# Kernel tuning notes

Hardware: AMD Instinct MI355X
Metric: run time of the kernel (lower is better)

The kernel has to match this reference:

```python
import jax, jax.numpy as jnp
import numpy as np

N = 30000
E = 480000
C_IN, H = 16, 4
NEG_SLOPE = 0.2  # PyG GATv2Conv default negative_slope


def gatv2(x, src, dst, Wl, bl, Wr, br, att, bias, heads, outc, concat, n):
    # PyG GATv2Conv (share_weights=False): e_ij = att . leaky_relu(Wl x_j + Wr x_i)
    xl = (x @ Wl + bl).reshape(n, heads, outc)   # source transform
    xr = (x @ Wr + br).reshape(n, heads, outc)   # target transform
    e = jax.nn.leaky_relu(xl[src] + xr[dst], NEG_SLOPE)        # [E,H,C]
    logits = jnp.einsum('ehc,hc->eh', e, att)                  # [E,H]
    m = jax.lax.stop_gradient(jax.ops.segment_max(logits, dst, num_segments=n))
    ex = jnp.exp(logits - m[dst])
    denom = jax.ops.segment_sum(ex, dst, num_segments=n)
    alpha = ex / denom[dst]                                    # scatter-softmax over in-edges
    out = jax.ops.segment_sum(alpha[:, :, None] * xl[src], dst, num_segments=n)  # [N,H,C]
    out = out.reshape(n, heads * outc) if concat else out.mean(axis=1)
    return out + bias


def setup_inputs() -> dict:
    key = jax.random.key(0)
    ks = jax.random.split(key, 16)
    s = 0.05
    inp = {
        'x': jax.random.uniform(ks[0], (N, C_IN), dtype=jnp.float32),
        'edge_index': jax.random.randint(ks[1], (2, E), 0, N, dtype=jnp.int32),
        'lower_bound': jnp.zeros((C_IN,), jnp.float32),
        'upper_bound': jnp.ones((C_IN,), jnp.float32),
        # Layer 1: GATv2Conv(16 -> 32 per head, heads=4, concat=True) => 128
        'W1l': jax.random.normal(ks[2], (C_IN, H * 32), jnp.float32) * s,
        'b1l': jnp.zeros((H * 32,), jnp.float32),
        'W1r': jax.random.normal(ks[3], (C_IN, H * 32), jnp.float32) * s,
        'b1r': jnp.zeros((H * 32,), jnp.float32),
        'att1': jax.random.normal(ks[4], (H, 32), jnp.float32) * s,
        'bias1': jnp.zeros((H * 32,), jnp.float32),
        # Layer 2: GATv2Conv(128 -> 64 per head, heads=4, concat=False) => 64
        'W2l': jax.random.normal(ks[5], (128, H * 64), jnp.float32) * s,
        'b2l': jnp.zeros((H * 64,), jnp.float32),
        'W2r': jax.random.normal(ks[6], (128, H * 64), jnp.float32) * s,
        'b2r': jnp.zeros((H * 64,), jnp.float32),
        'att2': jax.random.normal(ks[7], (H, 64), jnp.float32) * s,
        'bias2': jnp.zeros((64,), jnp.float32),
        # Final linear head 64 -> 5
        'W3': jax.random.normal(ks[8], (64, 5), jnp.float32) * s,
        'b3': jnp.zeros((5,), jnp.float32),
    }
    return inp


def reference(x, edge_index, lower_bound, upper_bound,
              W1l, b1l, W1r, b1r, att1, bias1,
              W2l, b2l, W2r, b2r, att2, bias2,
              W3, b3):
    n = x.shape[0]
    # min-max normalization
    y = (x - lower_bound) / (upper_bound - lower_bound)
    # add self loops (PyG GATv2Conv default add_self_loops=True)
    loops = jnp.tile(jnp.arange(n, dtype=edge_index.dtype)[None, :], (2, 1))
    ei = jnp.concatenate([edge_index, loops], axis=1)
    src, dst = ei[0], ei[1]
    y = gatv2(y, src, dst, W1l, b1l, W1r, b1r, att1, bias1, H, 32, True, n)
    y = jax.nn.relu(y)
    y = gatv2(y, src, dst, W2l, b2l, W2r, b2r, att2, bias2, H, 64, False, n)
    y = jax.nn.relu(y)
    y = y @ W3 + b3
    return jax.nn.sigmoid(y)
```

## Files before the change

kernel.cpp:

```cpp
#include <hip/hip_runtime.h>

#define H 4
#define D1 128
#define D2 256
#define CIN 16
#define SLOPE 0.2f
#define LOG2E 1.4426950408889634f

typedef short short8v __attribute__((ext_vector_type(8)));
typedef float float4v __attribute__((ext_vector_type(4)));
typedef float float2v __attribute__((ext_vector_type(2)));

__device__ __forceinline__ float bflo(unsigned u) { return __uint_as_float(u << 16); }
__device__ __forceinline__ float bfdirty(unsigned u) { return __uint_as_float(u); }
__device__ __forceinline__ unsigned short f2bf(float f) {
    unsigned int u = __float_as_uint(f);
    u += 0x7FFFu + ((u >> 16) & 1u);
    return (unsigned short)(u >> 16);
}
__device__ __forceinline__ unsigned short f2fp8x2(float a, float b) {
    return (unsigned short)__builtin_amdgcn_cvt_pk_fp8_f32(a, b, 0, false);
}

__device__ __forceinline__ float dpp_sum16(float x) {
    float t;
    t = __int_as_float(__builtin_amdgcn_mov_dpp(__float_as_int(x), 0xB1, 0xF, 0xF, true));
    x += t;
    t = __int_as_float(__builtin_amdgcn_mov_dpp(__float_as_int(x), 0x4E, 0xF, 0xF, true));
    x += t;
    t = __int_as_float(__builtin_amdgcn_mov_dpp(__float_as_int(x), 0x141, 0xF, 0xF, true));
    x += t;
    t = __int_as_float(__builtin_amdgcn_mov_dpp(__float_as_int(x), 0x140, 0xF, 0xF, true));
    x += t;
    return x;
}

__global__ void k_hist(const int* __restrict__ ei, int E, int ET,
                       int* __restrict__ deg) {
    int idx = blockIdx.x * blockDim.x + threadIdx.x;
    if (idx >= ET) return;
    int dst = (idx < E) ? ei[E + idx] : idx - E;
    atomicAdd(&deg[dst], 1);
}

__global__ __launch_bounds__(1024) void k_scan_one(
        const int* __restrict__ deg, int* __restrict__ rp,
        int* __restrict__ cur, int n) {
    __shared__ int wsum[16];
    int t = threadIdx.x;
    int lane = t & 63, w = t >> 6;
    int base = t * 32;
    int vals[32];
    const int4* dp = (const int4*)deg;
#pragma unroll
    for (int q = 0; q < 8; ++q) {
        int4 v = dp[(base >> 2) + q];
        vals[4 * q + 0] = v.x; vals[4 * q + 1] = v.y;
        vals[4 * q + 2] = v.z; vals[4 * q + 3] = v.w;
    }
    int loc[32];
    int s = 0;
#pragma unroll
    for (int k = 0; k < 32; ++k) {
        int idx = base + k;
        int v = (idx < n) ? vals[k] : 0;
        loc[k] = s;
        s += v;
    }
    int inc = s;
#pragma unroll
    for (int off = 1; off < 64; off <<= 1) {
        int u = __shfl_up(inc, off, 64);
        if (lane >= off) inc += u;
    }
    int excl = inc - s;
    if (lane == 63) wsum[w] = inc;
    __syncthreads();
    if (w == 0) {
        int v = (lane < 16) ? wsum[lane] : 0;
        int winc = v;
#pragma unroll
        for (int off = 1; off < 16; off <<= 1) {
            int u = __shfl_up(winc, off, 64);
            if (lane >= off) winc += u;
        }
        if (lane < 16) wsum[lane] = winc - v;
    }
    __syncthreads();
    int offw = wsum[w] + excl;
#pragma unroll
    for (int q = 0; q < 8; ++q) {
        int i0 = base + 4 * q;
        if (i0 + 3 < n) {
            *(int4*)(rp + i0) = make_int4(offw + loc[4 * q + 0], offw + loc[4 * q + 1],
                                          offw + loc[4 * q + 2], offw + loc[4 * q + 3]);
            *(int4*)(cur + i0) = make_int4(0, 0, 0, 0);
        } else {
#pragma unroll
            for (int e = 0; e < 4; ++e) {
                int idx = i0 + e;
                if (idx < n) { rp[idx] = offw + loc[4 * q + e]; cur[idx] = 0; }
            }
        }
    }
}

__global__ void k_fill(const int* __restrict__ ei, int E, int ET,
                       const int* __restrict__ rp, int* __restrict__ cur,
                       int* __restrict__ eord) {
    int idx = blockIdx.x * blockDim.x + threadIdx.x;
    if (idx >= ET) return;
    int src, dst;
    if (idx < E) { src = ei[idx]; dst = ei[E + idx]; }
    else         { src = dst = idx - E; }
    int pos = atomicAdd(&cur[dst], 1);
    eord[rp[dst] + pos] = src;
}

__global__ __launch_bounds__(256) void k_prep(
        const float* __restrict__ x, const float* __restrict__ lb,
        const float* __restrict__ ub,
        const float* __restrict__ Wl, const float* __restrict__ bl,
        const float* __restrict__ Wr, const float* __restrict__ br,
        unsigned char* __restrict__ xl8, float* __restrict__ xr,
        const float* __restrict__ W2l, const float* __restrict__ W2r,
        unsigned short* __restrict__ W2t,
        int* __restrict__ deg, int n, int B1) {
    __shared__ float Wls[CIN][D1];
    __shared__ float Wrs[CIN][D1];
    __shared__ float ys[16][CIN];
    int b = blockIdx.x;
    int t = threadIdx.x;
    if (b >= B1) {
        int rb = b - B1;
        if (rb < 256) {
            int idx = rb * 256 + t;
            int k = idx >> 9, c = idx & 511;
            float v = (c < 256) ? W2l[k * 256 + c] : W2r[k * 256 + (c - 256)];
            W2t[(size_t)c * 128 + k] = f2bf(v);
        } else {
            int idx = (rb - 256) * 256 + t;
            if (idx < n) deg[idx] = 0;
        }
        return;
    }
    int i0 = b * 16;
#pragma unroll
    for (int i = 0; i < 8; ++i) {
        int flat = t + 256 * i;
        int k = flat >> 7, c = flat & 127;
        Wls[k][c] = Wl[k * D1 + c];
        Wrs[k][c] = Wr[k * D1 + c];
    }
    {
        int node = t >> 4, k = t & 15;
        int gi = i0 + node;
        float xv = (gi < n) ? x[(size_t)gi * CIN + k] : 0.f;
        ys[node][k] = (xv - lb[k]) / (ub[k] - lb[k]);
    }
    __syncthreads();
    int c = t & 127;
    bool left = t < 128;
    const float (*Ws)[D1] = left ? Wls : Wrs;
    float bias = left ? bl[c] : br[c];
    for (int j = 0; j < 16; ++j) {
        float acc = bias;
#pragma unroll
        for (int k = 0; k < CIN; ++k) acc += ys[j][k] * Ws[k][c];
        int gi = i0 + j;
        float other = __shfl_xor(acc, 1);
        if (gi < n) {
            if (left) {
                if (!(c & 1))
                    *(unsigned short*)(xl8 + (size_t)gi * D1 + c) = f2fp8x2(acc, other);
            } else {
                xr[(size_t)gi * D1 + c] = acc;
            }
        }
    }
}

__global__ __launch_bounds__(256) void k_lin2_mfma(
        const unsigned short* __restrict__ h1b,
        const unsigned short* __restrict__ W2t,
        const float* __restrict__ b2l, const float* __restrict__ b2r,
        unsigned char* __restrict__ xl2,
        unsigned short* __restrict__ xr2,
        int n) {
    __shared__ unsigned short At[128 * 128];
    __shared__ unsigned short Bt[128 * 128];
    int t = threadIdx.x;
    int row0 = blockIdx.x * 128;
    int col0 = blockIdx.y * 128;

    {
        int r = t >> 1, hh = (t & 1) * 64;
        bool ok = (row0 + r) < n;
        const unsigned short* gA = h1b + (size_t)(row0 + r) * 128 + hh;
        const unsigned short* gB = W2t + (size_t)(col0 + r) * 128 + hh;
#pragma unroll
        for (int i = 0; i < 8; ++i) {
            uint4 vA = ok ? *(const uint4*)(gA + i * 8) : make_uint4(0, 0, 0, 0);
            uint4 vB = *(const uint4*)(gB + i * 8);
            int col = hh + i * 8;
            int idx = (r * 128 + col) ^ ((r & 15) << 3);
            *(uint4*)&At[idx] = vA;
            *(uint4*)&Bt[idx] = vB;
        }
    }
    __syncthreads();

    int w = t >> 6, l = t & 63;
    int wr = w >> 1, wc = w & 1;
    float4v acc[4][4];
#pragma unroll
    for (int m = 0; m < 4; ++m)
#pragma unroll
        for (int nn = 0; nn < 4; ++nn) acc[m][nn] = (float4v)0.f;

#pragma unroll
    for (int ks = 0; ks < 4; ++ks) {
        int kb = ks * 32 + ((l >> 4) << 3);
        short8v a[4], b[4];
#pragma unroll
        for (int m = 0; m < 4; ++m) {
            int r = wr * 64 + m * 16 + (l & 15);
            a[m] = *(const short8v*)&At[(r * 128 + kb) ^ ((r & 15) << 3)];
        }
#pragma unroll
        for (int nn = 0; nn < 4; ++nn) {
            int c = wc * 64 + nn * 16 + (l & 15);
            b[nn] = *(const short8v*)&Bt[(c * 128 + kb) ^ ((c & 15) << 3)];
        }
#pragma unroll
        for (int m = 0; m < 4; ++m)
#pragma unroll
            for (int nn = 0; nn < 4; ++nn)
                acc[m][nn] = __builtin_amdgcn_mfma_f32_16x16x32_bf16(
                    a[m], b[nn], acc[m][nn], 0, 0, 0);
    }

    if (col0 < 256) {
        const float* bp = b2l;
        int cb = col0;
#pragma unroll
        for (int nn = 0; nn < 4; ++nn) {
            int colc = cb + wc * 64 + nn * 16 + (l & 15);
            float bv = bp[colc];
#pragma unroll
            for (int m = 0; m < 4; ++m) {
                int rbase = row0 + wr * 64 + m * 16 + ((l >> 4) << 2);
#pragma unroll
                for (int r = 0; r < 4; ++r) {
                    int row = rbase + r;
                    float val = acc[m][nn][r] + bv;
                    float other = __shfl_xor(val, 1);
                    if (!(l & 1) && row < n)
                        *(unsigned short*)(xl2 + (size_t)row * 256 + colc) =
                            f2fp8x2(val, other);
                }
            }
        }
    } else {
        const float* bp = b2r;
        int cb = col0 - 256;
#pragma unroll
        for (int nn = 0; nn < 4; ++nn) {
            int colc = cb + wc * 64 + nn * 16 + (l & 15);
            float bv = bp[colc];
#pragma unroll
            for (int m = 0; m < 4; ++m) {
                int rbase = row0 + wr * 64 + m * 16 + ((l >> 4) << 2);
#pragma unroll
                for (int r = 0; r < 4; ++r) {
                    int row = rbase + r;
                    if (row < n)
                        xr2[(size_t)row * 256 + colc] = f2bf(acc[m][nn][r] + bv);
                }
            }
        }
    }
}

__global__ __launch_bounds__(256) void k_agg1(
        const unsigned char* __restrict__ xl8, const float* __restrict__ xr,
        const float* __restrict__ att, const float* __restrict__ bias,
        const int* __restrict__ rp, const int* __restrict__ deg,
        const int* __restrict__ eord, unsigned short* __restrict__ h1b, int n) {
    int t = threadIdx.x;
    int node = blockIdx.x * 4 + (t >> 6);
    int l = t & 63;
    int nd = (node < n) ? node : n - 1;
    float2 xrv = *(const float2*)(xr + (size_t)nd * D1 + 2 * l);
    float2 av  = *(const float2*)(att + 2 * l);
    av.x *= LOG2E; av.y *= LOG2E;
    int start = __builtin_amdgcn_readfirstlane(rp[nd]);
    int cnt   = (node < n) ? deg[nd] : 0;
    cnt = __builtin_amdgcn_readfirstlane(cnt);
    const unsigned short* xlp = (const unsigned short*)xl8;
    float d = 0.f, a0 = 0.f, a1 = 0.f;
    int cnt4 = cnt & ~3;
    unsigned r0, r1, r2, r3;
    if (cnt4 > 0) {
        int i0 = eord[start + 0], i1 = eord[start + 1];
        int i2 = eord[start + 2], i3 = eord[start + 3];
        r0 = xlp[(size_t)i0 * 64 + l]; r1 = xlp[(size_t)i1 * 64 + l];
        r2 = xlp[(size_t)i2 * 64 + l]; r3 = xlp[(size_t)i3 * 64 + l];
    }
    for (int j = 0; j < cnt4; j += 4) {
        unsigned p0 = r0, p1 = r1, p2 = r2, p3 = r3;
        int jn = j + 4;
        if (jn < cnt4) {
            int i0 = eord[start + jn + 0], i1 = eord[start + jn + 1];
            int i2 = eord[start + jn + 2], i3 = eord[start + jn + 3];
            r0 = xlp[(size_t)i0 * 64 + l]; r1 = xlp[(size_t)i1 * 64 + l];
            r2 = xlp[(size_t)i2 * 64 + l]; r3 = xlp[(size_t)i3 * 64 + l];
        }
        float2v f0 = __builtin_amdgcn_cvt_pk_f32_fp8(p0, false);
        float2v f1 = __builtin_amdgcn_cvt_pk_f32_fp8(p1, false);
        float2v f2 = __builtin_amdgcn_cvt_pk_f32_fp8(p2, false);
        float2v f3 = __builtin_amdgcn_cvt_pk_f32_fp8(p3, false);
        float v, lg0, lg1, lg2, lg3;
        v = f0.x + xrv.x; v = fmaxf(v, SLOPE * v); lg0  = av.x * v;
        v = f0.y + xrv.y; v = fmaxf(v, SLOPE * v); lg0 += av.y * v;
        v = f1.x + xrv.x; v = fmaxf(v, SLOPE * v); lg1  = av.x * v;
        v = f1.y + xrv.y; v = fmaxf(v, SLOPE * v); lg1 += av.y * v;
        v = f2.x + xrv.x; v = fmaxf(v, SLOPE * v); lg2  = av.x * v;
        v = f2.y + xrv.y; v = fmaxf(v, SLOPE * v); lg2 += av.y * v;
        v = f3.x + xrv.x; v = fmaxf(v, SLOPE * v); lg3  = av.x * v;
        v = f3.y + xrv.y; v = fmaxf(v, SLOPE * v); lg3 += av.y * v;
        lg0 = dpp_sum16(lg0); lg1 = dpp_sum16(lg1);
        lg2 = dpp_sum16(lg2); lg3 = dpp_sum16(lg3);
        float e0 = exp2f(lg0), e1 = exp2f(lg1);
        float e2 = exp2f(lg2), e3 = exp2f(lg3);
        d += (e0 + e1) + (e2 + e3);
        a0 += e0 * f0.x + e1 * f1.x + e2 * f2.x + e3 * f3.x;
        a1 += e0 * f0.y + e1 * f1.y + e2 * f2.y + e3 * f3.y;
    }
    for (int j = cnt4; j < cnt; ++j) {
        int s0 = eord[start + j];
        unsigned p0 = xlp[(size_t)s0 * 64 + l];
        float2v f0 = __builtin_amdgcn_cvt_pk_f32_fp8(p0, false);
        float v, lg0;
        v = f0.x + xrv.x; v = fmaxf(v, SLOPE * v); lg0  = av.x * v;
        v = f0.y + xrv.y; v = fmaxf(v, SLOPE * v); lg0 += av.y * v;
        lg0 = dpp_sum16(lg0);
        float e0 = exp2f(lg0);
        d += e0;
        a0 += e0 * f0.x;
        a1 += e0 * f0.y;
    }
    if (node < n) {
        float inv = 1.f / d;
        float o0 = fmaxf(a0 * inv + bias[2 * l + 0], 0.f);
        float o1 = fmaxf(a1 * inv + bias[2 * l + 1], 0.f);
        ((unsigned*)h1b)[(size_t)node * 64 + l] =
            ((unsigned)f2bf(o1) << 16) | f2bf(o0);
    }
}

__global__ __launch_bounds__(256) void k_agg2(
        const unsigned char* __restrict__ xl8, const unsigned short* __restrict__ xr,
        const float* __restrict__ att, const float* __restrict__ b2,
        const float* __restrict__ W3, const float* __restrict__ b3,
        const int* __restrict__ rp, const int* __restrict__ deg,
        const int* __restrict__ eord, float* __restrict__ out, int n) {
    int t = threadIdx.x;
    int node = blockIdx.x * 4 + (t >> 6);
    int l = t & 63;
    int nd = (node < n) ? node : n - 1;
    const uint2* xrp = (const uint2*)xr;
    uint2 xru = xrp[(size_t)nd * 64 + l];
    float4 xrv = make_float4(bflo(xru.x), bfdirty(xru.x), bflo(xru.y), bfdirty(xru.y));
    float4 av  = *(const float4*)(att + 4 * l);
    av.x *= LOG2E; av.y *= LOG2E; av.z *= LOG2E; av.w *= LOG2E;
    int start = __builtin_amdgcn_readfirstlane(rp[nd]);
    int cnt   = (node < n) ? deg[nd] : 0;
    cnt = __builtin_amdgcn_readfirstlane(cnt);
    const unsigned* xlp = (const unsigned*)xl8;
    float d = 0.f, a0 = 0.f, a1 = 0.f, a2 = 0.f, a3 = 0.f;
    int cnt4 = cnt & ~3;
    unsigned r0, r1, r2, r3;
    if (cnt4 > 0) {
        int i0 = eord[start + 0], i1 = eord[start + 1];
        int i2 = eord[start + 2], i3 = eord[start + 3];
        r0 = xlp[(size_t)i0 * 64 + l]; r1 = xlp[(size_t)i1 * 64 + l];
        r2 = xlp[(size_t)i2 * 64 + l]; r3 = xlp[(size_t)i3 * 64 + l];
    }
    for (int j = 0; j < cnt4; j += 4) {
        unsigned p0 = r0, p1 = r1, p2 = r2, p3 = r3;
        int jn = j + 4;
        if (jn < cnt4) {
            int i0 = eord[start + jn + 0], i1 = eord[start + jn + 1];
            int i2 = eord[start + jn + 2], i3 = eord[start + jn + 3];
            r0 = xlp[(size_t)i0 * 64 + l]; r1 = xlp[(size_t)i1 * 64 + l];
            r2 = xlp[(size_t)i2 * 64 + l]; r3 = xlp[(size_t)i3 * 64 + l];
        }
        float2v lo0 = __builtin_amdgcn_cvt_pk_f32_fp8(p0, false);
        float2v hi0 = __builtin_amdgcn_cvt_pk_f32_fp8(p0, true);
        float2v lo1 = __builtin_amdgcn_cvt_pk_f32_fp8(p1, false);
        float2v hi1 = __builtin_amdgcn_cvt_pk_f32_fp8(p1, true);
        float2v lo2 = __builtin_amdgcn_cvt_pk_f32_fp8(p2, false);
        float2v hi2 = __builtin_amdgcn_cvt_pk_f32_fp8(p2, true);
        float2v lo3 = __builtin_amdgcn_cvt_pk_f32_fp8(p3, false);
        float2v hi3 = __builtin_amdgcn_cvt_pk_f32_fp8(p3, true);
        float v, lg0, lg1, lg2, lg3;
        v = lo0.x + xrv.x; v = fmaxf(v, SLOPE * v); lg0  = av.x * v;
        v = lo0.y + xrv.y; v = fmaxf(v, SLOPE * v); lg0 += av.y * v;
        v = hi0.x + xrv.z; v = fmaxf(v, SLOPE * v); lg0 += av.z * v;
        v = hi0.y + xrv.w; v = fmaxf(v, SLOPE * v); lg0 += av.w * v;
        v = lo1.x + xrv.x; v = fmaxf(v, SLOPE * v); lg1  = av.x * v;
        v = lo1.y + xrv.y; v = fmaxf(v, SLOPE * v); lg1 += av.y * v;
        v = hi1.x + xrv.z; v = fmaxf(v, SLOPE * v); lg1 += av.z * v;
        v = hi1.y + xrv.w; v = fmaxf(v, SLOPE * v); lg1 += av.w * v;
        v = lo2.x + xrv.x; v = fmaxf(v, SLOPE * v); lg2  = av.x * v;
        v = lo2.y + xrv.y; v = fmaxf(v, SLOPE * v); lg2 += av.y * v;
        v = hi2.x + xrv.z; v = fmaxf(v, SLOPE * v); lg2 += av.z * v;
        v = hi2.y + xrv.w; v = fmaxf(v, SLOPE * v); lg2 += av.w * v;
        v = lo3.x + xrv.x; v = fmaxf(v, SLOPE * v); lg3  = av.x * v;
        v = lo3.y + xrv.y; v = fmaxf(v, SLOPE * v); lg3 += av.y * v;
        v = hi3.x + xrv.z; v = fmaxf(v, SLOPE * v); lg3 += av.z * v;
        v = hi3.y + xrv.w; v = fmaxf(v, SLOPE * v); lg3 += av.w * v;
        lg0 = dpp_sum16(lg0); lg1 = dpp_sum16(lg1);
        lg2 = dpp_sum16(lg2); lg3 = dpp_sum16(lg3);
        float e0 = exp2f(lg0), e1 = exp2f(lg1);
        float e2 = exp2f(lg2), e3 = exp2f(lg3);
        d += (e0 + e1) + (e2 + e3);
        a0 += e0 * lo0.x + e1 * lo1.x + e2 * lo2.x + e3 * lo3.x;
        a1 += e0 * lo0.y + e1 * lo1.y + e2 * lo2.y + e3 * lo3.y;
        a2 += e0 * hi0.x + e1 * hi1.x + e2 * hi2.x + e3 * hi3.x;
        a3 += e0 * hi0.y + e1 * hi1.y + e2 * hi2.y + e3 * hi3.y;
    }
    for (int j = cnt4; j < cnt; ++j) {
        int s0 = eord[start + j];
        unsigned p0 = xlp[(size_t)s0 * 64 + l];
        float2v lo0 = __builtin_amdgcn_cvt_pk_f32_fp8(p0, false);
        float2v hi0 = __builtin_amdgcn_cvt_pk_f32_fp8(p0, true);
        float v, lg0;
        v = lo0.x + xrv.x; v = fmaxf(v, SLOPE * v); lg0  = av.x * v;
        v = lo0.y + xrv.y; v = fmaxf(v, SLOPE * v); lg0 += av.y * v;
        v = hi0.x + xrv.z; v = fmaxf(v, SLOPE * v); lg0 += av.z * v;
        v = hi0.y + xrv.w; v = fmaxf(v, SLOPE * v); lg0 += av.w * v;
        lg0 = dpp_sum16(lg0);
        float e0 = exp2f(lg0);
        d += e0;
        a0 += e0 * lo0.x; a1 += e0 * lo0.y; a2 += e0 * hi0.x; a3 += e0 * hi0.y;
    }
    float inv = 1.f / d;
    float v0 = a0 * inv, v1 = a1 * inv, v2 = a2 * inv, v3 = a3 * inv;
    v0 += __shfl_xor(v0, 16); v1 += __shfl_xor(v1, 16);
    v2 += __shfl_xor(v2, 16); v3 += __shfl_xor(v3, 16);
    v0 += __shfl_xor(v0, 32); v1 += __shfl_xor(v1, 32);
    v2 += __shfl_xor(v2, 32); v3 += __shfl_xor(v3, 32);
    int c0 = 4 * (l & 15);
    v0 = fmaxf(0.25f * v0 + b2[c0 + 0], 0.f);
    v1 = fmaxf(0.25f * v1 + b2[c0 + 1], 0.f);
    v2 = fmaxf(0.25f * v2 + b2[c0 + 2], 0.f);
    v3 = fmaxf(0.25f * v3 + b2[c0 + 3], 0.f);
    float p0, p1, p2, p3, p4;
    {
        const float* w0 = W3 + (c0 + 0) * 5;
        const float* w1 = W3 + (c0 + 1) * 5;
        const float* w2 = W3 + (c0 + 2) * 5;
        const float* w3 = W3 + (c0 + 3) * 5;
        p0 = v0 * w0[0] + v1 * w1[0] + v2 * w2[0] + v3 * w3[0];
        p1 = v0 * w0[1] + v1 * w1[1] + v2 * w2[1] + v3 * w3[1];
        p2 = v0 * w0[2] + v1 * w1[2] + v2 * w2[2] + v3 * w3[2];
        p3 = v0 * w0[3] + v1 * w1[3] + v2 * w2[3] + v3 * w3[3];
        p4 = v0 * w0[4] + v1 * w1[4] + v2 * w2[4] + v3 * w3[4];
    }
    p0 = dpp_sum16(p0); p1 = dpp_sum16(p1); p2 = dpp_sum16(p2);
    p3 = dpp_sum16(p3); p4 = dpp_sum16(p4);
    if (l == 0 && node < n) {
        float* o = out + (size_t)node * 5;
        o[0] = 1.f / (1.f + __expf(-(p0 + b3[0])));
        o[1] = 1.f / (1.f + __expf(-(p1 + b3[1])));
        o[2] = 1.f / (1.f + __expf(-(p2 + b3[2])));
        o[3] = 1.f / (1.f + __expf(-(p3 + b3[3])));
        o[4] = 1.f / (1.f + __expf(-(p4 + b3[4])));
    }
}

extern "C" void kernel_launch(void* const* d_in, const int* in_sizes, int n_in,
                              void* d_out, int out_size, void* d_ws, size_t ws_size,
                              hipStream_t stream) {
    const float* x     = (const float*)d_in[0];
    const int*   ei    = (const int*)d_in[1];
    const float* lb    = (const float*)d_in[2];
    const float* ub    = (const float*)d_in[3];
    const float* W1l   = (const float*)d_in[4];
    const float* b1l   = (const float*)d_in[5];
    const float* W1r   = (const float*)d_in[6];
    const float* b1r   = (const float*)d_in[7];
    const float* att1  = (const float*)d_in[8];
    const float* bias1 = (const float*)d_in[9];
    const float* W2l   = (const float*)d_in[10];
    const float* b2l   = (const float*)d_in[11];
    const float* W2r   = (const float*)d_in[12];
    const float* b2r   = (const float*)d_in[13];
    const float* att2  = (const float*)d_in[14];
    const float* bias2 = (const float*)d_in[15];
    const float* W3    = (const float*)d_in[16];
    const float* b3    = (const float*)d_in[17];

    int n  = in_sizes[0] / CIN;
    int E  = in_sizes[1] / 2;
    int ET = E + n;

    char* ws = (char*)d_ws;
    size_t off = 0;
    auto alloc = [&](size_t nbytes) {
        void* p = ws + off;
        off += (nbytes + 255) & ~(size_t)255;
        return p;
    };
    unsigned char*  xl1 = (unsigned char*)alloc((size_t)n * D1);
    float*          xr1 = (float*)alloc((size_t)n * D1 * 4);
    unsigned short* h1b = (unsigned short*)alloc((size_t)n * D1 * 2);
    unsigned char*  xl2 = (unsigned char*)alloc((size_t)n * D2);
    unsigned short* xr2 = (unsigned short*)alloc((size_t)n * D2 * 2);
    unsigned short* W2t = (unsigned short*)alloc((size_t)512 * 128 * 2);
    int* deg  = (int*)alloc((size_t)n * 4 + 8192);
    int* cur  = (int*)alloc((size_t)n * 4);
    int* rp   = (int*)alloc((size_t)n * 4);
    int* eord = (int*)alloc((size_t)ET * 4);

    int B1 = (n + 15) / 16;
    int BZ = (n + 255) / 256;
    k_prep<<<B1 + 256 + BZ, 256, 0, stream>>>(
        x, lb, ub, W1l, b1l, W1r, b1r, xl1, xr1, W2l, W2r, W2t, deg, n, B1);

    k_hist<<<(ET + 255) / 256, 256, 0, stream>>>(ei, E, ET, deg);
    k_scan_one<<<1, 1024, 0, stream>>>(deg, rp, cur, n);
    k_fill<<<(ET + 255) / 256, 256, 0, stream>>>(ei, E, ET, rp, cur, eord);

    k_agg1<<<(n + 3) / 4, 256, 0, stream>>>(xl1, xr1, att1, bias1, rp, deg,
                                            eord, h1b, n);

    dim3 g2((n + 127) / 128, 4);
    k_lin2_mfma<<<g2, 256, 0, stream>>>(h1b, W2t, b2l, b2r, xl2, xr2, n);
    k_agg2<<<(n + 3) / 4, 256, 0, stream>>>(xl2, xr2, att2, bias2, W3, b3,
                                            rp, deg, eord, (float*)d_out, n);
}
```

Baseline: 182.4 us.

## Switch gather features from fp8 to fp16 and use packed half math in aggregation

```diff
diff --git a/kernel.cpp b/kernel.cpp
--- a/kernel.cpp
+++ b/kernel.cpp
@@ -9,17 +9,28 @@
 
 typedef short short8v __attribute__((ext_vector_type(8)));
 typedef float float4v __attribute__((ext_vector_type(4)));
-typedef float float2v __attribute__((ext_vector_type(2)));
-
-__device__ __forceinline__ float bflo(unsigned u) { return __uint_as_float(u << 16); }
-__device__ __forceinline__ float bfdirty(unsigned u) { return __uint_as_float(u); }
+typedef __fp16 half2v __attribute__((ext_vector_type(2)));
+
 __device__ __forceinline__ unsigned short f2bf(float f) {
     unsigned int u = __float_as_uint(f);
     u += 0x7FFFu + ((u >> 16) & 1u);
     return (unsigned short)(u >> 16);
 }
-__device__ __forceinline__ unsigned short f2fp8x2(float a, float b) {
-    return (unsigned short)__builtin_amdgcn_cvt_pk_fp8_f32(a, b, 0, false);
+__device__ __forceinline__ half2v pkrtz(float a, float b) {
+    return __builtin_amdgcn_cvt_pkrtz(a, b);
+}
+__device__ __forceinline__ half2v h2_from_u32(unsigned u) {
+    return __builtin_bit_cast(half2v, u);
+}
+__device__ __forceinline__ unsigned u32_from_h2(half2v h) {
+    return __builtin_bit_cast(unsigned, h);
+}
+__device__ __forceinline__ float fdot2(half2v a, half2v b, float c) {
+#if __has_builtin(__builtin_amdgcn_fdot2)
+    return __builtin_amdgcn_fdot2(a, b, c, false);
+#else
+    return c + (float)a.x * (float)b.x + (float)a.y * (float)b.y;
+#endif
 }
 
 __device__ __forceinline__ float dpp_sum16(float x) {
@@ -122,7 +133,7 @@
         const float* __restrict__ ub,
         const float* __restrict__ Wl, const float* __restrict__ bl,
         const float* __restrict__ Wr, const float* __restrict__ br,
-        unsigned char* __restrict__ xl8, float* __restrict__ xr,
+        unsigned short* __restrict__ xl16, unsigned short* __restrict__ xr16,
         const float* __restrict__ W2l, const float* __restrict__ W2r,
         unsigned short* __restrict__ W2t,
         int* __restrict__ deg, int n, int B1) {
@@ -163,20 +174,15 @@
     bool left = t < 128;
     const float (*Ws)[D1] = left ? Wls : Wrs;
     float bias = left ? bl[c] : br[c];
+    unsigned short* obuf = left ? xl16 : xr16;
     for (int j = 0; j < 16; ++j) {
         float acc = bias;
 #pragma unroll
         for (int k = 0; k < CIN; ++k) acc += ys[j][k] * Ws[k][c];
         int gi = i0 + j;
         float other = __shfl_xor(acc, 1);
-        if (gi < n) {
-            if (left) {
-                if (!(c & 1))
-                    *(unsigned short*)(xl8 + (size_t)gi * D1 + c) = f2fp8x2(acc, other);
-            } else {
-                xr[(size_t)gi * D1 + c] = acc;
-            }
-        }
+        if (gi < n && !(c & 1))
+            *(unsigned*)(obuf + (size_t)gi * D1 + c) = u32_from_h2(pkrtz(acc, other));
     }
 }
 
@@ -184,7 +190,7 @@
         const unsigned short* __restrict__ h1b,
         const unsigned short* __restrict__ W2t,
         const float* __restrict__ b2l, const float* __restrict__ b2r,
-        unsigned char* __restrict__ xl2,
+        unsigned short* __restrict__ xl2,
         unsigned short* __restrict__ xr2,
         int n) {
     __shared__ unsigned short At[128 * 128];
@@ -240,50 +246,31 @@
                     a[m], b[nn], acc[m][nn], 0, 0, 0);
     }
 
-    if (col0 < 256) {
-        const float* bp = b2l;
-        int cb = col0;
-#pragma unroll
-        for (int nn = 0; nn < 4; ++nn) {
-            int colc = cb + wc * 64 + nn * 16 + (l & 15);
-            float bv = bp[colc];
-#pragma unroll
-            for (int m = 0; m < 4; ++m) {
-                int rbase = row0 + wr * 64 + m * 16 + ((l >> 4) << 2);
-#pragma unroll
-                for (int r = 0; r < 4; ++r) {
-                    int row = rbase + r;
-                    float val = acc[m][nn][r] + bv;
-                    float other = __shfl_xor(val, 1);
-                    if (!(l & 1) && row < n)
-                        *(unsigned short*)(xl2 + (size_t)row * 256 + colc) =
-                            f2fp8x2(val, other);
-                }
+    unsigned short* ob = (col0 < 256) ? xl2 : xr2;
+    const float* bp = (col0 < 256) ? b2l : b2r;
+    int cb = (col0 < 256) ? col0 : col0 - 256;
+#pragma unroll
+    for (int nn = 0; nn < 4; ++nn) {
+        int colc = cb + wc * 64 + nn * 16 + (l & 15);
+        float bv = bp[colc];
+#pragma unroll
+        for (int m = 0; m < 4; ++m) {
+            int rbase = row0 + wr * 64 + m * 16 + ((l >> 4) << 2);
+#pragma unroll
+            for (int r = 0; r < 4; ++r) {
+                int row = rbase + r;
+                float val = acc[m][nn][r] + bv;
+                float other = __shfl_xor(val, 1);
+                if (!(l & 1) && row < n)
+                    *(unsigned*)(ob + (size_t)row * 256 + colc) =
+                        u32_from_h2(pkrtz(val, other));
             }
         }
-    } else {
-        const float* bp = b2r;
-        int cb = col0 - 256;
-#pragma unroll
-        for (int nn = 0; nn < 4; ++nn) {
-            int colc = cb + wc * 64 + nn * 16 + (l & 15);
-            float bv = bp[colc];
-#pragma unroll
-            for (int m = 0; m < 4; ++m) {
-                int rbase = row0 + wr * 64 + m * 16 + ((l >> 4) << 2);
-#pragma unroll
-                for (int r = 0; r < 4; ++r) {
-                    int row = rbase + r;
-                    if (row < n)
-                        xr2[(size_t)row * 256 + colc] = f2bf(acc[m][nn][r] + bv);
-                }
-            }
-        }
     }
 }
 
 __global__ __launch_bounds__(256) void k_agg1(
-        const unsigned char* __restrict__ xl8, const float* __restrict__ xr,
+        const unsigned short* __restrict__ xl16, const unsigned short* __restrict__ xr16,
         const float* __restrict__ att, const float* __restrict__ bias,
         const int* __restrict__ rp, const int* __restrict__ deg,
         const int* __restrict__ eord, unsigned short* __restrict__ h1b, int n) {
@@ -291,14 +278,16 @@
     int node = blockIdx.x * 4 + (t >> 6);
     int l = t & 63;
     int nd = (node < n) ? node : n - 1;
-    float2 xrv = *(const float2*)(xr + (size_t)nd * D1 + 2 * l);
-    float2 av  = *(const float2*)(att + 2 * l);
-    av.x *= LOG2E; av.y *= LOG2E;
+    half2v xr01 = h2_from_u32(((const unsigned*)xr16)[(size_t)nd * 64 + l]);
+    float2 av = *(const float2*)(att + 2 * l);
+    half2v av01 = pkrtz(av.x * LOG2E, av.y * LOG2E);
+    half2v slp = pkrtz(SLOPE, SLOPE);
     int start = __builtin_amdgcn_readfirstlane(rp[nd]);
     int cnt   = (node < n) ? deg[nd] : 0;
     cnt = __builtin_amdgcn_readfirstlane(cnt);
-    const unsigned short* xlp = (const unsigned short*)xl8;
-    float d = 0.f, a0 = 0.f, a1 = 0.f;
+    const unsigned* xlp = (const unsigned*)xl16;
+    float d = 0.f;
+    half2v a01 = pkrtz(0.f, 0.f);
     int cnt4 = cnt & ~3;
     unsigned r0, r1, r2, r3;
     if (cnt4 > 0) {
@@ -308,7 +297,8 @@
         r2 = xlp[(size_t)i2 * 64 + l]; r3 = xlp[(size_t)i3 * 64 + l];
     }
     for (int j = 0; j < cnt4; j += 4) {
-        unsigned p0 = r0, p1 = r1, p2 = r2, p3 = r3;
+        half2v x0 = h2_from_u32(r0), x1 = h2_from_u32(r1);
+        half2v x2 = h2_from_u32(r2), x3 = h2_from_u32(r3);
         int jn = j + 4;
         if (jn < cnt4) {
             int i0 = eord[start + jn + 0], i1 = eord[start + jn + 1];
@@ -316,51 +306,47 @@
             r0 = xlp[(size_t)i0 * 64 + l]; r1 = xlp[(size_t)i1 * 64 + l];
             r2 = xlp[(size_t)i2 * 64 + l]; r3 = xlp[(size_t)i3 * 64 + l];
         }
-        float2v f0 = __builtin_amdgcn_cvt_pk_f32_fp8(p0, false);
-        float2v f1 = __builtin_amdgcn_cvt_pk_f32_fp8(p1, false);
-        float2v f2 = __builtin_amdgcn_cvt_pk_f32_fp8(p2, false);
-        float2v f3 = __builtin_amdgcn_cvt_pk_f32_fp8(p3, false);
-        float v, lg0, lg1, lg2, lg3;
-        v = f0.x + xrv.x; v = fmaxf(v, SLOPE * v); lg0  = av.x * v;
-        v = f0.y + xrv.y; v = fmaxf(v, SLOPE * v); lg0 += av.y * v;
-        v = f1.x + xrv.x; v = fmaxf(v, SLOPE * v); lg1  = av.x * v;
-        v = f1.y + xrv.y; v = fmaxf(v, SLOPE * v); lg1 += av.y * v;
-        v = f2.x + xrv.x; v = fmaxf(v, SLOPE * v); lg2  = av.x * v;
-        v = f2.y + xrv.y; v = fmaxf(v, SLOPE * v); lg2 += av.y * v;
-        v = f3.x + xrv.x; v = fmaxf(v, SLOPE * v); lg3  = av.x * v;
-        v = f3.y + xrv.y; v = fmaxf(v, SLOPE * v); lg3 += av.y * v;
+        half2v s0 = x0 + xr01, s1 = x1 + xr01, s2 = x2 + xr01, s3 = x3 + xr01;
+        s0 = __builtin_elementwise_max(s0, s0 * slp);
+        s1 = __builtin_elementwise_max(s1, s1 * slp);
+        s2 = __builtin_elementwise_max(s2, s2 * slp);
+        s3 = __builtin_elementwise_max(s3, s3 * slp);
+        float lg0 = fdot2(av01, s0, 0.f);
+        float lg1 = fdot2(av01, s1, 0.f);
+        float lg2 = fdot2(av01, s2, 0.f);
+        float lg3 = fdot2(av01, s3, 0.f);
         lg0 = dpp_sum16(lg0); lg1 = dpp_sum16(lg1);
         lg2 = dpp_sum16(lg2); lg3 = dpp_sum16(lg3);
         float e0 = exp2f(lg0), e1 = exp2f(lg1);
         float e2 = exp2f(lg2), e3 = exp2f(lg3);
         d += (e0 + e1) + (e2 + e3);
-        a0 += e0 * f0.x + e1 * f1.x + e2 * f2.x + e3 * f3.x;
-        a1 += e0 * f0.y + e1 * f1.y + e2 * f2.y + e3 * f3.y;
+        a01 += pkrtz(e0, e0) * x0;
+        a01 += pkrtz(e1, e1) * x1;
+        a01 += pkrtz(e2, e2) * x2;
+        a01 += pkrtz(e3, e3) * x3;
     }
     for (int j = cnt4; j < cnt; ++j) {
-        int s0 = eord[start + j];
-        unsigned p0 = xlp[(size_t)s0 * 64 + l];
-        float2v f0 = __builtin_amdgcn_cvt_pk_f32_fp8(p0, false);
-        float v, lg0;
-        v = f0.x + xrv.x; v = fmaxf(v, SLOPE * v); lg0  = av.x * v;
-        v = f0.y + xrv.y; v = fmaxf(v, SLOPE * v); lg0 += av.y * v;
+        int s0i = eord[start + j];
+        half2v x0 = h2_from_u32(xlp[(size_t)s0i * 64 + l]);
+        half2v s0 = x0 + xr01;
+        s0 = __builtin_elementwise_max(s0, s0 * slp);
+        float lg0 = fdot2(av01, s0, 0.f);
         lg0 = dpp_sum16(lg0);
         float e0 = exp2f(lg0);
         d += e0;
-        a0 += e0 * f0.x;
-        a1 += e0 * f0.y;
+        a01 += pkrtz(e0, e0) * x0;
     }
     if (node < n) {
         float inv = 1.f / d;
-        float o0 = fmaxf(a0 * inv + bias[2 * l + 0], 0.f);
-        float o1 = fmaxf(a1 * inv + bias[2 * l + 1], 0.f);
+        float o0 = fmaxf((float)a01.x * inv + bias[2 * l + 0], 0.f);
+        float o1 = fmaxf((float)a01.y * inv + bias[2 * l + 1], 0.f);
         ((unsigned*)h1b)[(size_t)node * 64 + l] =
             ((unsigned)f2bf(o1) << 16) | f2bf(o0);
     }
 }
 
 __global__ __launch_bounds__(256) void k_agg2(
-        const unsigned char* __restrict__ xl8, const unsigned short* __restrict__ xr,
+        const unsigned short* __restrict__ xl16, const unsigned short* __restrict__ xr16,
         const float* __restrict__ att, const float* __restrict__ b2,
         const float* __restrict__ W3, const float* __restrict__ b3,
         const int* __restrict__ rp, const int* __restrict__ deg,
@@ -369,18 +355,20 @@
     int node = blockIdx.x * 4 + (t >> 6);
     int l = t & 63;
     int nd = (node < n) ? node : n - 1;
-    const uint2* xrp = (const uint2*)xr;
-    uint2 xru = xrp[(size_t)nd * 64 + l];
-    float4 xrv = make_float4(bflo(xru.x), bfdirty(xru.x), bflo(xru.y), bfdirty(xru.y));
-    float4 av  = *(const float4*)(att + 4 * l);
-    av.x *= LOG2E; av.y *= LOG2E; av.z *= LOG2E; av.w *= LOG2E;
+    uint2 xru = ((const uint2*)xr16)[(size_t)nd * 64 + l];
+    half2v xr01 = h2_from_u32(xru.x), xr23 = h2_from_u32(xru.y);
+    float4 av = *(const float4*)(att + 4 * l);
+    half2v av01 = pkrtz(av.x * LOG2E, av.y * LOG2E);
+    half2v av23 = pkrtz(av.z * LOG2E, av.w * LOG2E);
+    half2v slp = pkrtz(SLOPE, SLOPE);
     int start = __builtin_amdgcn_readfirstlane(rp[nd]);
     int cnt   = (node < n) ? deg[nd] : 0;
     cnt = __builtin_amdgcn_readfirstlane(cnt);
-    const unsigned* xlp = (const unsigned*)xl8;
-    float d = 0.f, a0 = 0.f, a1 = 0.f, a2 = 0.f, a3 = 0.f;
+    const uint2* xlp = (const uint2*)xl16;
+    float d = 0.f;
+    half2v a01 = pkrtz(0.f, 0.f), a23 = pkrtz(0.f, 0.f);
     int cnt4 = cnt & ~3;
-    unsigned r0, r1, r2, r3;
+    uint2 r0, r1, r2, r3;
     if (cnt4 > 0) {
         int i0 = eord[start + 0], i1 = eord[start + 1];
         int i2 = eord[start + 2], i3 = eord[start + 3];
@@ -388,7 +376,10 @@
         r2 = xlp[(size_t)i2 * 64 + l]; r3 = xlp[(size_t)i3 * 64 + l];
     }
     for (int j = 0; j < cnt4; j += 4) {
-        unsigned p0 = r0, p1 = r1, p2 = r2, p3 = r3;
+        half2v x00 = h2_from_u32(r0.x), x01p = h2_from_u32(r0.y);
+        half2v x10 = h2_from_u32(r1.x), x11p = h2_from_u32(r1.y);
+        half2v x20 = h2_from_u32(r2.x), x21p = h2_from_u32(r2.y);
+        half2v x30 = h2_from_u32(r3.x), x31p = h2_from_u32(r3.y);
         int jn = j + 4;
         if (jn < cnt4) {
             int i0 = eord[start + jn + 0], i1 = eord[start + jn + 1];
@@ -396,58 +387,54 @@
             r0 = xlp[(size_t)i0 * 64 + l]; r1 = xlp[(size_t)i1 * 64 + l];
             r2 = xlp[(size_t)i2 * 64 + l]; r3 = xlp[(size_t)i3 * 64 + l];
         }
-        float2v lo0 = __builtin_amdgcn_cvt_pk_f32_fp8(p0, false);
-        float2v hi0 = __builtin_amdgcn_cvt_pk_f32_fp8(p0, true);
-        float2v lo1 = __builtin_amdgcn_cvt_pk_f32_fp8(p1, false);
-        float2v hi1 = __builtin_amdgcn_cvt_pk_f32_fp8(p1, true);
-        float2v lo2 = __builtin_amdgcn_cvt_pk_f32_fp8(p2, false);
-        float2v hi2 = __builtin_amdgcn_cvt_pk_f32_fp8(p2, true);
-        float2v lo3 = __builtin_amdgcn_cvt_pk_f32_fp8(p3, false);
-        float2v hi3 = __builtin_amdgcn_cvt_pk_f32_fp8(p3, true);
-        float v, lg0, lg1, lg2, lg3;
-        v = lo0.x + xrv.x; v = fmaxf(v, SLOPE * v); lg0  = av.x * v;
-        v = lo0.y + xrv.y; v = fmaxf(v, SLOPE * v); lg0 += av.y * v;
-        v = hi0.x + xrv.z; v = fmaxf(v, SLOPE * v); lg0 += av.z * v;
-        v = hi0.y + xrv.w; v = fmaxf(v, SLOPE * v); lg0 += av.w * v;
-        v = lo1.x + xrv.x; v = fmaxf(v, SLOPE * v); lg1  = av.x * v;
-        v = lo1.y + xrv.y; v = fmaxf(v, SLOPE * v); lg1 += av.y * v;
-        v = hi1.x + xrv.z; v = fmaxf(v, SLOPE * v); lg1 += av.z * v;
-        v = hi1.y + xrv.w; v = fmaxf(v, SLOPE * v); lg1 += av.w * v;
-        v = lo2.x + xrv.x; v = fmaxf(v, SLOPE * v); lg2  = av.x * v;
-        v = lo2.y + xrv.y; v = fmaxf(v, SLOPE * v); lg2 += av.y * v;
-        v = hi2.x + xrv.z; v = fmaxf(v, SLOPE * v); lg2 += av.z * v;
-        v = hi2.y + xrv.w; v = fmaxf(v, SLOPE * v); lg2 += av.w * v;
-        v = lo3.x + xrv.x; v = fmaxf(v, SLOPE * v); lg3  = av.x * v;
-        v = lo3.y + xrv.y; v = fmaxf(v, SLOPE * v); lg3 += av.y * v;
-        v = hi3.x + xrv.z; v = fmaxf(v, SLOPE * v); lg3 += av.z * v;
-        v = hi3.y + xrv.w; v = fmaxf(v, SLOPE * v); lg3 += av.w * v;
+        half2v s;
+        float lg0, lg1, lg2, lg3;
+        s = x00 + xr01; s = __builtin_elementwise_max(s, s * slp);
+        lg0 = fdot2(av01, s, 0.f);
+        s = x01p + xr23; s = __builtin_elementwise_max(s, s * slp);
+        lg0 = fdot2(av23, s, lg0);
+        s = x10 + xr01; s = __builtin_elementwise_max(s, s * slp);
+        lg1 = fdot2(av01, s, 0.f);
+        s = x11p + xr23; s = __builtin_elementwise_max(s, s * slp);
+        lg1 = fdot2(av23, s, lg1);
+        s = x20 + xr01; s = __builtin_elementwise_max(s, s * slp);
+        lg2 = fdot2(av01, s, 0.f);
+        s = x21p + xr23; s = __builtin_elementwise_max(s, s * slp);
+        lg2 = fdot2(av23, s, lg2);
+        s = x30 + xr01; s = __builtin_elementwise_max(s, s * slp);
+        lg3 = fdot2(av01, s, 0.f);
+        s = x31p + xr23; s = __builtin_elementwise_max(s, s * slp);
+        lg3 = fdot2(av23, s, lg3);
         lg0 = dpp_sum16(lg0); lg1 = dpp_sum16(lg1);
         lg2 = dpp_sum16(lg2); lg3 = dpp_sum16(lg3);
         float e0 = exp2f(lg0), e1 = exp2f(lg1);
         float e2 = exp2f(lg2), e3 = exp2f(lg3);
         d += (e0 + e1) + (e2 + e3);
-        a0 += e0 * lo0.x + e1 * lo1.x + e2 * lo2.x + e3 * lo3.x;
-        a1 += e0 * lo0.y + e1 * lo1.y + e2 * lo2.y + e3 * lo3.y;
-        a2 += e0 * hi0.x + e1 * hi1.x + e2 * hi2.x + e3 * hi3.x;
-        a3 += e0 * hi0.y + e1 * hi1.y + e2 * hi2.y + e3 * hi3.y;
+        half2v ep;
+        ep = pkrtz(e0, e0); a01 += ep * x00; a23 += ep * x01p;
+        ep = pkrtz(e1, e1); a01 += ep * x10; a23 += ep * x11p;
+        ep = pkrtz(e2, e2); a01 += ep * x20; a23 += ep * x21p;
+        ep = pkrtz(e3, e3); a01 += ep * x30; a23 += ep * x31p;
     }
     for (int j = cnt4; j < cnt; ++j) {
-        int s0 = eord[start + j];
-        unsigned p0 = xlp[(size_t)s0 * 64 + l];
-        float2v lo0 = __builtin_amdgcn_cvt_pk_f32_fp8(p0, false);
-        float2v hi0 = __builtin_amdgcn_cvt_pk_f32_fp8(p0, true);
-        float v, lg0;
-        v = lo0.x + xrv.x; v = fmaxf(v, SLOPE * v); lg0  = av.x * v;
-        v = lo0.y + xrv.y; v = fmaxf(v, SLOPE * v); lg0 += av.y * v;
-        v = hi0.x + xrv.z; v = fmaxf(v, SLOPE * v); lg0 += av.z * v;
-        v = hi0.y + xrv.w; v = fmaxf(v, SLOPE * v); lg0 += av.w * v;
+        int s0i = eord[start + j];
+        uint2 p0 = xlp[(size_t)s0i * 64 + l];
+        half2v x00 = h2_from_u32(p0.x), x01p = h2_from_u32(p0.y);
+        half2v s;
+        float lg0;
+        s = x00 + xr01; s = __builtin_elementwise_max(s, s * slp);
+        lg0 = fdot2(av01, s, 0.f);
+        s = x01p + xr23; s = __builtin_elementwise_max(s, s * slp);
+        lg0 = fdot2(av23, s, lg0);
         lg0 = dpp_sum16(lg0);
         float e0 = exp2f(lg0);
         d += e0;
-        a0 += e0 * lo0.x; a1 += e0 * lo0.y; a2 += e0 * hi0.x; a3 += e0 * hi0.y;
+        half2v ep = pkrtz(e0, e0);
+        a01 += ep * x00; a23 += ep * x01p;
     }
     float inv = 1.f / d;
-    float v0 = a0 * inv, v1 = a1 * inv, v2 = a2 * inv, v3 = a3 * inv;
+    float v0 = (float)a01.x * inv, v1 = (float)a01.y * inv;
+    float v2 = (float)a23.x * inv, v3 = (float)a23.y * inv;
     v0 += __shfl_xor(v0, 16); v1 += __shfl_xor(v1, 16);
     v2 += __shfl_xor(v2, 16); v3 += __shfl_xor(v3, 16);
     v0 += __shfl_xor(v0, 32); v1 += __shfl_xor(v1, 32);
@@ -514,10 +501,10 @@
         off += (nbytes + 255) & ~(size_t)255;
         return p;
     };
-    unsigned char*  xl1 = (unsigned char*)alloc((size_t)n * D1);
-    float*          xr1 = (float*)alloc((size_t)n * D1 * 4);
+    unsigned short* xl1 = (unsigned short*)alloc((size_t)n * D1 * 2);
+    unsigned short* xr1 = (unsigned short*)alloc((size_t)n * D1 * 2);
     unsigned short* h1b = (unsigned short*)alloc((size_t)n * D1 * 2);
-    unsigned char*  xl2 = (unsigned char*)alloc((size_t)n * D2);
+    unsigned short* xl2 = (unsigned short*)alloc((size_t)n * D2 * 2);
     unsigned short* xr2 = (unsigned short*)alloc((size_t)n * D2 * 2);
     unsigned short* W2t = (unsigned short*)alloc((size_t)512 * 128 * 2);
     int* deg  = (int*)alloc((size_t)n * 4 + 8192);
```

New measurement: 171.6 us. -5.9%, faster.
